# Performance work log

Measured on AMD Instinct MI355X. Metric: run time of the kernel, lower is better.

## Reference

```python
import jax, jax.numpy as jnp
import numpy as np

N = 50000
E = 800000
IN_C = 128
HID = 64
HEADS = 4
EPS = 1e-5
NEG_SLOPE = 0.2


def _glorot(key, shape, fan_in):
    return jax.random.normal(key, shape, dtype=jnp.float32) / np.sqrt(fan_in)


def setup_inputs() -> dict:
    key = jax.random.key(0)
    ks = jax.random.split(key, 32)
    d = {}
    d["x"] = jax.random.normal(ks[0], (N, IN_C), dtype=jnp.float32)
    d["edge_index"] = jax.random.randint(ks[1], (2, E), 0, N, dtype=jnp.int32)
    ph = HID // HEADS  # per-head channels for concat layers (16)
    # Layer 1: in -> [heads, ph], concat
    d["W1"] = _glorot(ks[2], (IN_C, HEADS * ph), IN_C)
    d["a1s"] = _glorot(ks[3], (HEADS, ph), ph)
    d["a1d"] = _glorot(ks[4], (HEADS, ph), ph)
    d["b1"] = jnp.zeros((HID,), jnp.float32)
    # Layer 2: hid -> [heads, ph], concat
    d["W2"] = _glorot(ks[5], (HID, HEADS * ph), HID)
    d["a2s"] = _glorot(ks[6], (HEADS, ph), ph)
    d["a2d"] = _glorot(ks[7], (HEADS, ph), ph)
    d["b2"] = jnp.zeros((HID,), jnp.float32)
    # Layer 3: hid -> [heads, HID], mean over heads (concat=False)
    d["W3"] = _glorot(ks[8], (HID, HEADS * HID), HID)
    d["a3s"] = _glorot(ks[9], (HEADS, HID), HID)
    d["a3d"] = _glorot(ks[10], (HEADS, HID), HID)
    d["b3"] = jnp.zeros((HID,), jnp.float32)
    # BatchNorms (eval mode: running stats)
    for i, k0 in zip((1, 2, 3), (11, 14, 17)):
        d[f"bn{i}_g"] = jnp.ones((HID,), jnp.float32)
        d[f"bn{i}_b"] = jnp.zeros((HID,), jnp.float32)
        d[f"bn{i}_m"] = 0.1 * jax.random.normal(ks[k0], (HID,), dtype=jnp.float32)
        d[f"bn{i}_v"] = jax.random.uniform(ks[k0 + 1], (HID,), minval=0.5, maxval=1.5, dtype=jnp.float32)
    # Classifier MLP: HID -> HID//2 -> 1
    d["cW1"] = _glorot(ks[20], (HID, HID // 2), HID)
    d["cb1"] = jnp.zeros((HID // 2,), jnp.float32)
    d["cW2"] = _glorot(ks[21], (HID // 2, 1), HID // 2)
    d["cb2"] = jnp.zeros((1,), jnp.float32)
    return d


def _gat_layer(x, src, dst, W, a_s, a_d, b, concat):
    n = x.shape[0]
    heads, outc = a_s.shape
    h = (x @ W).reshape(n, heads, outc)           # [N,H,C]
    al_s = jnp.einsum("nhc,hc->nh", h, a_s)       # [N,H]
    al_d = jnp.einsum("nhc,hc->nh", h, a_d)
    e = jax.nn.leaky_relu(al_s[src] + al_d[dst], NEG_SLOPE)  # [E,H]
    m = jax.ops.segment_max(e, dst, num_segments=n)
    ex = jnp.exp(e - m[dst])
    den = jax.ops.segment_sum(ex, dst, num_segments=n)
    alpha = ex / den[dst]                          # segment softmax over dst
    out = jax.ops.segment_sum(h[src] * alpha[..., None], dst, num_segments=n)  # [N,H,C]
    if concat:
        out = out.reshape(n, heads * outc)
    else:
        out = out.mean(axis=1)
    return out + b


def _bn(x, g, b, m, v):
    return g * (x - m) * jax.lax.rsqrt(v + EPS) + b


def reference(x, edge_index, W1, a1s, a1d, b1, W2, a2s, a2d, b2, W3, a3s, a3d, b3,
              bn1_g, bn1_b, bn1_m, bn1_v, bn2_g, bn2_b, bn2_m, bn2_v,
              bn3_g, bn3_b, bn3_m, bn3_v, cW1, cb1, cW2, cb2):
    n = x.shape[0]
    # PyG GATConv adds self-loops by default
    loop = jnp.arange(n, dtype=edge_index.dtype)
    src = jnp.concatenate([edge_index[0], loop])
    dst = jnp.concatenate([edge_index[1], loop])

    h = _gat_layer(x, src, dst, W1, a1s, a1d, b1, concat=True)
    h = jax.nn.elu(_bn(h, bn1_g, bn1_b, bn1_m, bn1_v))
    h = _gat_layer(h, src, dst, W2, a2s, a2d, b2, concat=True)
    h = jax.nn.elu(_bn(h, bn2_g, bn2_b, bn2_m, bn2_v))
    h = _gat_layer(h, src, dst, W3, a3s, a3d, b3, concat=False)
    h = _bn(h, bn3_g, bn3_b, bn3_m, bn3_v)

    h = jax.nn.elu(h @ cW1 + cb1)
    out = (h @ cW2 + cb2).squeeze(-1)  # [N]
    return out
```

## Files before the change

kernel.cpp:

```cpp
#include <hip/hip_runtime.h>

#define HH 4

__device__ __forceinline__ float lrelu(float v){ return v > 0.f ? v : 0.2f*v; }

template<int IC>
__global__ void gemm_gat(const float* __restrict__ X, const float* __restrict__ W,
                         const float* __restrict__ a_s, const float* __restrict__ a_d,
                         float* __restrict__ h, float* __restrict__ als, float* __restrict__ ald,
                         int N) {
    int t = threadIdx.x, lane = t & 63, wid = t >> 6;
    int n = blockIdx.x*4 + wid;
    bool valid = n < N;
    int nc = valid ? n : N-1;
    __shared__ float xs[4][IC];
    #pragma unroll
    for (int k = lane; k < IC; k += 64) xs[wid][k] = X[(size_t)nc*IC + k];
    float acc = 0.f;
    #pragma unroll 8
    for (int k = 0; k < IC; ++k) acc += xs[wid][k] * W[k*64 + lane];
    if (valid) h[(size_t)nc*64 + lane] = acc;
    int hh = lane >> 4, c = lane & 15;
    float ps = acc * a_s[hh*16 + c];
    float pd = acc * a_d[hh*16 + c];
    #pragma unroll
    for (int m = 1; m < 16; m <<= 1){ ps += __shfl_xor(ps, m); pd += __shfl_xor(pd, m); }
    if (valid && c == 0){ als[nc*HH + hh] = ps; ald[nc*HH + hh] = pd; }
}


__global__ void zero_i32(int* __restrict__ p, int n){
    int i = blockIdx.x*256 + threadIdx.x;
    if (i < n) p[i] = 0;
}

__global__ void count_deg(const int* __restrict__ ei, int* __restrict__ deg, int E){
    int e = blockIdx.x*256 + threadIdx.x;
    if (e < E) atomicAdd(&deg[ei[E + e]], 1);
}

__global__ void deg_bsum(const int* __restrict__ deg, int* __restrict__ bsum, int N){
    int t = threadIdx.x;
    int base = blockIdx.x*1024 + t*4;
    int s = 0;
    if (base + 3 < N){
        int4 v = *(const int4*)(deg + base);
        s = v.x + v.y + v.z + v.w;
    } else {
        for (int q = 0; q < 4; ++q) if (base + q < N) s += deg[base + q];
    }
    #pragma unroll
    for (int m = 1; m < 64; m <<= 1) s += __shfl_xor(s, m);
    __shared__ int ws[4];
    if ((t & 63) == 0) ws[t >> 6] = s;
    __syncthreads();
    if (t == 0) bsum[blockIdx.x] = ws[0] + ws[1] + ws[2] + ws[3];
}

__global__ void scan_write(const int* __restrict__ deg, const int* __restrict__ bsum,
                           int* __restrict__ row_off, int* __restrict__ cursor, int N, int E){
    int t = threadIdx.x, bid = blockIdx.x, lane = t & 63, w = t >> 6;
    int base = bid*1024 + t*4;
    int v0 = 0, v1 = 0, v2 = 0, v3 = 0;
    if (base + 3 < N){
        int4 v = *(const int4*)(deg + base);
        v0 = v.x; v1 = v.y; v2 = v.z; v3 = v.w;
    } else {
        if (base     < N) v0 = deg[base];
        if (base + 1 < N) v1 = deg[base + 1];
        if (base + 2 < N) v2 = deg[base + 2];
        if (base + 3 < N) v3 = deg[base + 3];
    }
    int s = v0 + v1 + v2 + v3;
    int x = s;
    #pragma unroll
    for (int d = 1; d < 64; d <<= 1){
        int y = __shfl_up(x, d);
        if (lane >= d) x += y;
    }
    __shared__ int wsum[4];
    __shared__ int boff_s;
    if (lane == 63) wsum[w] = x;
    if (t < 64){
        int o = 0;
        for (int i = t; i < bid; i += 64) o += bsum[i];
        #pragma unroll
        for (int m = 1; m < 64; m <<= 1) o += __shfl_xor(o, m);
        if (t == 0) boff_s = o;
    }
    __syncthreads();
    int woff = 0;
    for (int i = 0; i < w; ++i) woff += wsum[i];
    int o = boff_s + woff + (x - s);
    if (base     < N){ row_off[base]     = o; cursor[base]     = o; o += v0; }
    if (base + 1 < N){ row_off[base + 1] = o; cursor[base + 1] = o; o += v1; }
    if (base + 2 < N){ row_off[base + 2] = o; cursor[base + 2] = o; o += v2; }
    if (base + 3 < N){ row_off[base + 3] = o; cursor[base + 3] = o; o += v3; }
    if (t == 0 && bid == 0) row_off[N] = E;
}

__global__ void fill_csr(const int* __restrict__ ei, int* __restrict__ cursor,
                         int* __restrict__ ssrc, int E){
    int e = blockIdx.x*256 + threadIdx.x;
    if (e < E){
        int d = ei[E + e];
        int p = atomicAdd(&cursor[d], 1);
        ssrc[p] = ei[e];
    }
}

__global__ void prep_l3(const float* __restrict__ W3, const float* __restrict__ a3s,
                        const float* __restrict__ a3d, float* __restrict__ ws3,
                        float* __restrict__ wd3, float* __restrict__ W3p){
    int t = threadIdx.x;
    int hh = t >> 6, k = t & 63;
    float ss = 0.f, sd = 0.f;
    for (int c = 0; c < 64; ++c){
        float w = W3[k*256 + hh*64 + c];
        ss += w * a3s[hh*64 + c];
        sd += w * a3d[hh*64 + c];
        W3p[t*64 + c] = 0.25f * w;
    }
    ws3[t] = ss; wd3[t] = sd;
}

template<bool L3PREP>
__global__ void gat_agg16(const int* __restrict__ row_off, const int* __restrict__ ssrc,
                          const float* __restrict__ als, const float* __restrict__ ald,
                          const float* __restrict__ h, const float* __restrict__ b,
                          const float* __restrict__ g, const float* __restrict__ bb,
                          const float* __restrict__ bm, const float* __restrict__ bv,
                          float* __restrict__ out,
                          const float* __restrict__ ws3, const float* __restrict__ wd3,
                          float* __restrict__ als3, float* __restrict__ ald3, int N){
    int lane = threadIdx.x & 63;
    int n = blockIdx.x*4 + (threadIdx.x >> 6);
    if (n >= N) return;
    int hh = lane >> 4, j = lane & 15, grp = lane & 48;
    float ad = ald[n*HH + hh];
    float vself = __expf(lrelu(als[n*HH + hh] + ad));
    int beg = row_off[n], end = row_off[n+1];
    float denp = 0.f;
    float acc = vself * h[(size_t)n*64 + lane];
    for (int cb = beg; cb < end; cb += 16){
        int e = cb + j;
        int s = n; float ev = 0.f;
        if (e < end){ s = ssrc[e]; ev = __expf(lrelu(als[s*HH + hh] + ad)); }
        denp += ev;
        #pragma unroll
        for (int qb = 0; qb < 16; qb += 8){
            int sq[8]; float hv[8];
            #pragma unroll
            for (int i = 0; i < 8; ++i) sq[i] = __shfl(s, grp | (qb + i));
            #pragma unroll
            for (int i = 0; i < 8; ++i) hv[i] = h[(size_t)sq[i]*64 + lane];
            #pragma unroll
            for (int i = 0; i < 8; ++i) acc += __shfl(ev, grp | (qb + i)) * hv[i];
        }
    }
    #pragma unroll
    for (int m = 1; m < 16; m <<= 1) denp += __shfl_xor(denp, m);
    float den = vself + denp;
    float val = acc/den + b[lane];
    val = g[lane]*(val - bm[lane])*rsqrtf(bv[lane] + 1e-5f) + bb[lane];
    val = val > 0.f ? val : expm1f(val);
    out[(size_t)n*64 + lane] = val;
    if (L3PREP){
        #pragma unroll
        for (int jj = 0; jj < 4; ++jj){
            float ps = val * ws3[jj*64 + lane];
            float pd = val * wd3[jj*64 + lane];
            #pragma unroll
            for (int mm = 1; mm < 64; mm <<= 1){
                ps += __shfl_xor(ps, mm);
                pd += __shfl_xor(pd, mm);
            }
            if (lane == 0){ als3[n*HH + jj] = ps; ald3[n*HH + jj] = pd; }
        }
    }
}

__global__ void gat_agg3_fused(const int* __restrict__ row_off, const int* __restrict__ ssrc,
                               const float* __restrict__ als, const float* __restrict__ ald,
                               const float* __restrict__ hin, const float* __restrict__ W3p,
                               const float* __restrict__ b, const float* __restrict__ g,
                               const float* __restrict__ bb, const float* __restrict__ bm,
                               const float* __restrict__ bv, float* __restrict__ out, int N){
    int t = threadIdx.x, lane = t & 63, wid = t >> 6;
    int n0 = blockIdx.x*4;
    int n = min(n0 + wid, N-1);
    __shared__ __align__(16) float4 wlds[4][64];
    __shared__ int slds[4][64];
    __shared__ __align__(16) float ysh[4*256];
    __shared__ float red[4][4][64];
    float4 adv = *(const float4*)(ald + n*4);
    float4 av  = *(const float4*)(als + n*4);
    float v0 = __expf(lrelu(av.x + adv.x)), v1 = __expf(lrelu(av.y + adv.y));
    float v2 = __expf(lrelu(av.z + adv.z)), v3 = __expf(lrelu(av.w + adv.w));
    int beg = row_off[n], end = row_off[n+1];
    float hv0 = hin[(size_t)n*64 + lane];
    float acc0 = v0*hv0, acc1 = v1*hv0, acc2 = v2*hv0, acc3 = v3*hv0;
    float dp0 = 0.f, dp1 = 0.f, dp2 = 0.f, dp3 = 0.f;
    for (int cb = beg; cb < end; cb += 64){
        int e = cb + lane;
        int s = n; float e0 = 0.f, e1 = 0.f, e2 = 0.f, e3 = 0.f;
        if (e < end){
            s = ssrc[e];
            float4 a = *(const float4*)(als + s*4);
            e0 = __expf(lrelu(a.x + adv.x));
            e1 = __expf(lrelu(a.y + adv.y));
            e2 = __expf(lrelu(a.z + adv.z));
            e3 = __expf(lrelu(a.w + adv.w));
        }
        dp0 += e0; dp1 += e1; dp2 += e2; dp3 += e3;
        wlds[wid][lane] = make_float4(e0, e1, e2, e3);
        slds[wid][lane] = s;
        int cn = min(64, end - cb);
        for (int qb = 0; qb < cn; qb += 8){
            int sq[8]; float hv[8]; float4 wv[8];
            #pragma unroll
            for (int i = 0; i < 8; ++i) sq[i] = slds[wid][qb + i];
            #pragma unroll
            for (int i = 0; i < 8; ++i) hv[i] = hin[(size_t)sq[i]*64 + lane];
            #pragma unroll
            for (int i = 0; i < 8; ++i) wv[i] = wlds[wid][qb + i];
            #pragma unroll
            for (int i = 0; i < 8; ++i){
                acc0 += wv[i].x*hv[i];
                acc1 += wv[i].y*hv[i];
                acc2 += wv[i].z*hv[i];
                acc3 += wv[i].w*hv[i];
            }
        }
    }
    #pragma unroll
    for (int m = 1; m < 64; m <<= 1){
        dp0 += __shfl_xor(dp0, m); dp1 += __shfl_xor(dp1, m);
        dp2 += __shfl_xor(dp2, m); dp3 += __shfl_xor(dp3, m);
    }
    ysh[wid*256 +   0 + lane] = acc0/(v0 + dp0);
    ysh[wid*256 +  64 + lane] = acc1/(v1 + dp1);
    ysh[wid*256 + 128 + lane] = acc2/(v2 + dp2);
    ysh[wid*256 + 192 + lane] = acc3/(v3 + dp3);
    __syncthreads();
    float a0 = 0.f, a1 = 0.f, a2 = 0.f, a3 = 0.f;
    int jbase = wid*64;
    #pragma unroll 4
    for (int jj = 0; jj < 64; jj += 4){
        int jb = jbase + jj;
        float4 y0 = *(const float4*)&ysh[0*256 + jb];
        float4 y1 = *(const float4*)&ysh[1*256 + jb];
        float4 y2 = *(const float4*)&ysh[2*256 + jb];
        float4 y3 = *(const float4*)&ysh[3*256 + jb];
        float w0 = W3p[(jb    )*64 + lane];
        float w1 = W3p[(jb + 1)*64 + lane];
        float w2 = W3p[(jb + 2)*64 + lane];
        float w3 = W3p[(jb + 3)*64 + lane];
        a0 += y0.x*w0 + y0.y*w1 + y0.z*w2 + y0.w*w3;
        a1 += y1.x*w0 + y1.y*w1 + y1.z*w2 + y1.w*w3;
        a2 += y2.x*w0 + y2.y*w1 + y2.z*w2 + y2.w*w3;
        a3 += y3.x*w0 + y3.y*w1 + y3.z*w2 + y3.w*w3;
    }
    red[wid][0][lane] = a0;
    red[wid][1][lane] = a1;
    red[wid][2][lane] = a2;
    red[wid][3][lane] = a3;
    __syncthreads();
    int nw = n0 + wid;
    if (nw < N){
        float val = red[0][wid][lane] + red[1][wid][lane] +
                    red[2][wid][lane] + red[3][wid][lane] + b[lane];
        out[(size_t)nw*64 + lane] = g[lane]*(val - bm[lane])*rsqrtf(bv[lane] + 1e-5f) + bb[lane];
    }
}

__global__ void classifier(const float* __restrict__ hin, const float* __restrict__ cW1,
                           const float* __restrict__ cb1, const float* __restrict__ cW2,
                           const float* __restrict__ cb2, float* __restrict__ out, int N){
    __shared__ float w1[64*32];
    __shared__ float b1s[32], w2[32];
    int t = threadIdx.x;
    for (int k = t; k < 64*32; k += 256) w1[k] = cW1[k];
    if (t < 32) { b1s[t] = cb1[t]; w2[t] = cW2[t]; }
    __syncthreads();
    int n = blockIdx.x*256 + t;
    if (n >= N) return;
    float hrow[64];
    #pragma unroll
    for (int k = 0; k < 64; ++k) hrow[k] = hin[(size_t)n*64 + k];
    float acc2 = cb2[0];
    #pragma unroll 4
    for (int j = 0; j < 32; ++j) {
        float a = b1s[j];
        #pragma unroll
        for (int k = 0; k < 64; ++k) a += hrow[k]*w1[k*32 + j];
        float e = a > 0.f ? a : expm1f(a);
        acc2 += e * w2[j];
    }
    out[n] = acc2;
}

extern "C" void kernel_launch(void* const* d_in, const int* in_sizes, int n_in,
                              void* d_out, int out_size, void* d_ws, size_t ws_size,
                              hipStream_t stream) {
    const float* x    = (const float*)d_in[0];
    const int*   ei   = (const int*)  d_in[1];
    const float* W1   = (const float*)d_in[2];
    const float* a1s  = (const float*)d_in[3];
    const float* a1d  = (const float*)d_in[4];
    const float* b1   = (const float*)d_in[5];
    const float* W2   = (const float*)d_in[6];
    const float* a2s  = (const float*)d_in[7];
    const float* a2d  = (const float*)d_in[8];
    const float* b2   = (const float*)d_in[9];
    const float* W3   = (const float*)d_in[10];
    const float* a3s  = (const float*)d_in[11];
    const float* a3d  = (const float*)d_in[12];
    const float* b3   = (const float*)d_in[13];
    const float* bn1g = (const float*)d_in[14];
    const float* bn1b = (const float*)d_in[15];
    const float* bn1m = (const float*)d_in[16];
    const float* bn1v = (const float*)d_in[17];
    const float* bn2g = (const float*)d_in[18];
    const float* bn2b = (const float*)d_in[19];
    const float* bn2m = (const float*)d_in[20];
    const float* bn2v = (const float*)d_in[21];
    const float* bn3g = (const float*)d_in[22];
    const float* bn3b = (const float*)d_in[23];
    const float* bn3m = (const float*)d_in[24];
    const float* bn3v = (const float*)d_in[25];
    const float* cW1  = (const float*)d_in[26];
    const float* cb1  = (const float*)d_in[27];
    const float* cW2  = (const float*)d_in[28];
    const float* cb2  = (const float*)d_in[29];

    const int N = in_sizes[0] / 128;
    const int E = in_sizes[1] / 2;

    float* h    = (float*)d_ws;
    float* hin  = h    + (size_t)N*64;
    float* als  = hin  + (size_t)N*64;
    float* ald  = als  + (size_t)N*4;
    float* als3 = ald  + (size_t)N*4;
    float* ald3 = als3 + (size_t)N*4;
    float* ws3  = ald3 + (size_t)N*4;
    float* wd3  = ws3  + 256;
    float* W3p  = wd3  + 256;
    int* deg     = (int*)(W3p + 16384);
    int* row_off = deg + N;
    int* cursor  = row_off + (N + 1);
    int* ssrc    = cursor + N;
    int* bsum    = ssrc + E;

    const int B = 256;
    int gN  = (N + B-1)/B;
    int gE  = (E + B-1)/B;
    int NB  = (N + 1023)/1024;
    int gN4 = (N + 3)/4;

    zero_i32<<<gN, B, 0, stream>>>(deg, N);
    count_deg<<<gE, B, 0, stream>>>(ei, deg, E);
    deg_bsum<<<NB, B, 0, stream>>>(deg, bsum, N);
    scan_write<<<NB, B, 0, stream>>>(deg, bsum, row_off, cursor, N, E);
    fill_csr<<<gE, B, 0, stream>>>(ei, cursor, ssrc, E);
    prep_l3<<<1, 256, 0, stream>>>(W3, a3s, a3d, ws3, wd3, W3p);

    gemm_gat<128><<<gN4, B, 0, stream>>>(x, W1, a1s, a1d, h, als, ald, N);
    gat_agg16<false><<<gN4, B, 0, stream>>>(row_off, ssrc, als, ald, h, b1,
                                            bn1g, bn1b, bn1m, bn1v, hin,
                                            nullptr, nullptr, nullptr, nullptr, N);

    gemm_gat<64><<<gN4, B, 0, stream>>>(hin, W2, a2s, a2d, h, als, ald, N);
    gat_agg16<true><<<gN4, B, 0, stream>>>(row_off, ssrc, als, ald, h, b2,
                                           bn2g, bn2b, bn2m, bn2v, hin,
                                           ws3, wd3, als3, ald3, N);

    gat_agg3_fused<<<gN4, B, 0, stream>>>(row_off, ssrc, als3, ald3, hin, W3p,
                                          b3, bn3g, bn3b, bn3m, bn3v, h, N);

    classifier<<<gN, B, 0, stream>>>(h, cW1, cb1, cW2, cb2, (float*)d_out, N);
}
```

Before: 401.6 us.

## Gather neighbor features as float4 with four edges per wavefront in parallel

The aggregation kernels for layers 1/2 and layer 3 now split each wavefront into four 16-lane groups. Each group loads a different neighbor's 64-float row as float4 vectors, so four edges are processed at once instead of one edge per 64-lane row load. Partial accumulators are combined afterwards with cross-group shuffles. The aim is fewer, wider gather instructions and more memory-level parallelism, at the cost of extra shuffle reductions and LDS staging of edge weights.

```diff
diff --git a/kernel.cpp b/kernel.cpp
--- a/kernel.cpp
+++ b/kernel.cpp
@@ -133,50 +133,74 @@
                           float* __restrict__ out,
                           const float* __restrict__ ws3, const float* __restrict__ wd3,
                           float* __restrict__ als3, float* __restrict__ ald3, int N){
-    int lane = threadIdx.x & 63;
-    int n = blockIdx.x*4 + (threadIdx.x >> 6);
+    int t = threadIdx.x, lane = t & 63, wid = t >> 6;
+    int n = blockIdx.x*4 + wid;
     if (n >= N) return;
-    int hh = lane >> 4, j = lane & 15, grp = lane & 48;
-    float ad = ald[n*HH + hh];
-    float vself = __expf(lrelu(als[n*HH + hh] + ad));
+    __shared__ float wl[4][16][4];
+    __shared__ int   sl[4][16];
+    int j  = lane & 15;
+    int hh = lane >> 4;
+    int cb = lane & 15;
+    int gq = lane >> 4;
+    int hd = cb >> 2;
+    float ad_w = ald[n*HH + hh];
+    float v_hd = __expf(lrelu(als[n*HH + hd] + ald[n*HH + hd]));
     int beg = row_off[n], end = row_off[n+1];
+    float4 acc = make_float4(0.f, 0.f, 0.f, 0.f);
+    if (lane < 16){
+        float4 hs = *(const float4*)(h + (size_t)n*64 + cb*4);
+        acc.x = v_hd*hs.x; acc.y = v_hd*hs.y; acc.z = v_hd*hs.z; acc.w = v_hd*hs.w;
+    }
     float denp = 0.f;
-    float acc = vself * h[(size_t)n*64 + lane];
-    for (int cb = beg; cb < end; cb += 16){
-        int e = cb + j;
+    for (int c16 = beg; c16 < end; c16 += 16){
+        int e = c16 + j;
         int s = n; float ev = 0.f;
-        if (e < end){ s = ssrc[e]; ev = __expf(lrelu(als[s*HH + hh] + ad)); }
+        if (e < end){ s = ssrc[e]; ev = __expf(lrelu(als[s*HH + hh] + ad_w)); }
         denp += ev;
+        wl[wid][j][hh] = ev;
+        if (hh == 0) sl[wid][j] = s;
+        int cnt = min(16, end - c16);
+        for (int qb = 0; qb < cnt; qb += 8){
+            int eA = qb + gq, eB = qb + 4 + gq;
+            int   sA = sl[wid][eA],     sB = sl[wid][eB];
+            float wA = wl[wid][eA][hd], wB = wl[wid][eB][hd];
+            float4 hA = *(const float4*)(h + (size_t)sA*64 + cb*4);
+            float4 hB = *(const float4*)(h + (size_t)sB*64 + cb*4);
+            acc.x += wA*hA.x; acc.y += wA*hA.y; acc.z += wA*hA.z; acc.w += wA*hA.w;
+            acc.x += wB*hB.x; acc.y += wB*hB.y; acc.z += wB*hB.z; acc.w += wB*hB.w;
+        }
+    }
+    #pragma unroll
+    for (int m = 1; m < 16; m <<= 1) denp += __shfl_xor(denp, m);
+    float den = __shfl(denp, hd << 4) + v_hd;
+    #pragma unroll
+    for (int m = 16; m < 64; m <<= 1){
+        acc.x += __shfl_xor(acc.x, m); acc.y += __shfl_xor(acc.y, m);
+        acc.z += __shfl_xor(acc.z, m); acc.w += __shfl_xor(acc.w, m);
+    }
+    float4 bb4 = *(const float4*)(b  + cb*4);
+    float4 gg4 = *(const float4*)(g  + cb*4);
+    float4 be4 = *(const float4*)(bb + cb*4);
+    float4 bm4 = *(const float4*)(bm + cb*4);
+    float4 bv4 = *(const float4*)(bv + cb*4);
+    float4 val;
+    val.x = gg4.x*(acc.x/den + bb4.x - bm4.x)*rsqrtf(bv4.x + 1e-5f) + be4.x;
+    val.y = gg4.y*(acc.y/den + bb4.y - bm4.y)*rsqrtf(bv4.y + 1e-5f) + be4.y;
+    val.z = gg4.z*(acc.z/den + bb4.z - bm4.z)*rsqrtf(bv4.z + 1e-5f) + be4.z;
+    val.w = gg4.w*(acc.w/den + bb4.w - bm4.w)*rsqrtf(bv4.w + 1e-5f) + be4.w;
+    val.x = val.x > 0.f ? val.x : expm1f(val.x);
+    val.y = val.y > 0.f ? val.y : expm1f(val.y);
+    val.z = val.z > 0.f ? val.z : expm1f(val.z);
+    val.w = val.w > 0.f ? val.w : expm1f(val.w);
+    if (lane < 16) *(float4*)(out + (size_t)n*64 + cb*4) = val;
+    if (L3PREP){
+        float4 w_s = *(const float4*)(ws3 + gq*64 + cb*4);
+        float4 w_d = *(const float4*)(wd3 + gq*64 + cb*4);
+        float ps = val.x*w_s.x + val.y*w_s.y + val.z*w_s.z + val.w*w_s.w;
+        float pd = val.x*w_d.x + val.y*w_d.y + val.z*w_d.z + val.w*w_d.w;
         #pragma unroll
-        for (int qb = 0; qb < 16; qb += 8){
-            int sq[8]; float hv[8];
-            #pragma unroll
-            for (int i = 0; i < 8; ++i) sq[i] = __shfl(s, grp | (qb + i));
-            #pragma unroll
-            for (int i = 0; i < 8; ++i) hv[i] = h[(size_t)sq[i]*64 + lane];
-            #pragma unroll
-            for (int i = 0; i < 8; ++i) acc += __shfl(ev, grp | (qb + i)) * hv[i];
-        }
-    }
-    #pragma unroll
-    for (int m = 1; m < 16; m <<= 1) denp += __shfl_xor(denp, m);
-    float den = vself + denp;
-    float val = acc/den + b[lane];
-    val = g[lane]*(val - bm[lane])*rsqrtf(bv[lane] + 1e-5f) + bb[lane];
-    val = val > 0.f ? val : expm1f(val);
-    out[(size_t)n*64 + lane] = val;
-    if (L3PREP){
-        #pragma unroll
-        for (int jj = 0; jj < 4; ++jj){
-            float ps = val * ws3[jj*64 + lane];
-            float pd = val * wd3[jj*64 + lane];
-            #pragma unroll
-            for (int mm = 1; mm < 64; mm <<= 1){
-                ps += __shfl_xor(ps, mm);
-                pd += __shfl_xor(pd, mm);
-            }
-            if (lane == 0){ als3[n*HH + jj] = ps; ald3[n*HH + jj] = pd; }
-        }
+        for (int m = 1; m < 16; m <<= 1){ ps += __shfl_xor(ps, m); pd += __shfl_xor(pd, m); }
+        if (cb == 0){ als3[n*HH + gq] = ps; ald3[n*HH + gq] = pd; }
     }
 }
 
@@ -193,16 +217,23 @@
     __shared__ int slds[4][64];
     __shared__ __align__(16) float ysh[4*256];
     __shared__ float red[4][4][64];
+    int cb = lane & 15, gq = lane >> 4;
     float4 adv = *(const float4*)(ald + n*4);
     float4 av  = *(const float4*)(als + n*4);
     float v0 = __expf(lrelu(av.x + adv.x)), v1 = __expf(lrelu(av.y + adv.y));
     float v2 = __expf(lrelu(av.z + adv.z)), v3 = __expf(lrelu(av.w + adv.w));
     int beg = row_off[n], end = row_off[n+1];
-    float hv0 = hin[(size_t)n*64 + lane];
-    float acc0 = v0*hv0, acc1 = v1*hv0, acc2 = v2*hv0, acc3 = v3*hv0;
+    float4 acc0 = make_float4(0,0,0,0), acc1 = acc0, acc2 = acc0, acc3 = acc0;
+    if (lane < 16){
+        float4 hs = *(const float4*)(hin + (size_t)n*64 + cb*4);
+        acc0.x = v0*hs.x; acc0.y = v0*hs.y; acc0.z = v0*hs.z; acc0.w = v0*hs.w;
+        acc1.x = v1*hs.x; acc1.y = v1*hs.y; acc1.z = v1*hs.z; acc1.w = v1*hs.w;
+        acc2.x = v2*hs.x; acc2.y = v2*hs.y; acc2.z = v2*hs.z; acc2.w = v2*hs.w;
+        acc3.x = v3*hs.x; acc3.y = v3*hs.y; acc3.z = v3*hs.z; acc3.w = v3*hs.w;
+    }
     float dp0 = 0.f, dp1 = 0.f, dp2 = 0.f, dp3 = 0.f;
-    for (int cb = beg; cb < end; cb += 64){
-        int e = cb + lane;
+    for (int c64 = beg; c64 < end; c64 += 64){
+        int e = c64 + lane;
         int s = n; float e0 = 0.f, e1 = 0.f, e2 = 0.f, e3 = 0.f;
         if (e < end){
             s = ssrc[e];
@@ -215,22 +246,21 @@
         dp0 += e0; dp1 += e1; dp2 += e2; dp3 += e3;
         wlds[wid][lane] = make_float4(e0, e1, e2, e3);
         slds[wid][lane] = s;
-        int cn = min(64, end - cb);
+        int cn = min(64, end - c64);
         for (int qb = 0; qb < cn; qb += 8){
-            int sq[8]; float hv[8]; float4 wv[8];
-            #pragma unroll
-            for (int i = 0; i < 8; ++i) sq[i] = slds[wid][qb + i];
-            #pragma unroll
-            for (int i = 0; i < 8; ++i) hv[i] = hin[(size_t)sq[i]*64 + lane];
-            #pragma unroll
-            for (int i = 0; i < 8; ++i) wv[i] = wlds[wid][qb + i];
-            #pragma unroll
-            for (int i = 0; i < 8; ++i){
-                acc0 += wv[i].x*hv[i];
-                acc1 += wv[i].y*hv[i];
-                acc2 += wv[i].z*hv[i];
-                acc3 += wv[i].w*hv[i];
-            }
+            int eA = qb + gq, eB = qb + 4 + gq;
+            int sA = slds[wid][eA], sB = slds[wid][eB];
+            float4 wA = wlds[wid][eA], wB = wlds[wid][eB];
+            float4 hA = *(const float4*)(hin + (size_t)sA*64 + cb*4);
+            float4 hB = *(const float4*)(hin + (size_t)sB*64 + cb*4);
+            acc0.x += wA.x*hA.x; acc0.y += wA.x*hA.y; acc0.z += wA.x*hA.z; acc0.w += wA.x*hA.w;
+            acc1.x += wA.y*hA.x; acc1.y += wA.y*hA.y; acc1.z += wA.y*hA.z; acc1.w += wA.y*hA.w;
+            acc2.x += wA.z*hA.x; acc2.y += wA.z*hA.y; acc2.z += wA.z*hA.z; acc2.w += wA.z*hA.w;
+            acc3.x += wA.w*hA.x; acc3.y += wA.w*hA.y; acc3.z += wA.w*hA.z; acc3.w += wA.w*hA.w;
+            acc0.x += wB.x*hB.x; acc0.y += wB.x*hB.y; acc0.z += wB.x*hB.z; acc0.w += wB.x*hB.w;
+            acc1.x += wB.y*hB.x; acc1.y += wB.y*hB.y; acc1.z += wB.y*hB.z; acc1.w += wB.y*hB.w;
+            acc2.x += wB.z*hB.x; acc2.y += wB.z*hB.y; acc2.z += wB.z*hB.z; acc2.w += wB.z*hB.w;
+            acc3.x += wB.w*hB.x; acc3.y += wB.w*hB.y; acc3.z += wB.w*hB.z; acc3.w += wB.w*hB.w;
         }
     }
     #pragma unroll
@@ -238,10 +268,29 @@
         dp0 += __shfl_xor(dp0, m); dp1 += __shfl_xor(dp1, m);
         dp2 += __shfl_xor(dp2, m); dp3 += __shfl_xor(dp3, m);
     }
-    ysh[wid*256 +   0 + lane] = acc0/(v0 + dp0);
-    ysh[wid*256 +  64 + lane] = acc1/(v1 + dp1);
-    ysh[wid*256 + 128 + lane] = acc2/(v2 + dp2);
-    ysh[wid*256 + 192 + lane] = acc3/(v3 + dp3);
+    #pragma unroll
+    for (int m = 16; m < 64; m <<= 1){
+        acc0.x += __shfl_xor(acc0.x, m); acc0.y += __shfl_xor(acc0.y, m);
+        acc0.z += __shfl_xor(acc0.z, m); acc0.w += __shfl_xor(acc0.w, m);
+        acc1.x += __shfl_xor(acc1.x, m); acc1.y += __shfl_xor(acc1.y, m);
+        acc1.z += __shfl_xor(acc1.z, m); acc1.w += __shfl_xor(acc1.w, m);
+        acc2.x += __shfl_xor(acc2.x, m); acc2.y += __shfl_xor(acc2.y, m);
+        acc2.z += __shfl_xor(acc2.z, m); acc2.w += __shfl_xor(acc2.w, m);
+        acc3.x += __shfl_xor(acc3.x, m); acc3.y += __shfl_xor(acc3.y, m);
+        acc3.z += __shfl_xor(acc3.z, m); acc3.w += __shfl_xor(acc3.w, m);
+    }
+    if (lane < 16){
+        float r0 = 1.f/(v0 + dp0), r1 = 1.f/(v1 + dp1);
+        float r2 = 1.f/(v2 + dp2), r3 = 1.f/(v3 + dp3);
+        float4 y0 = make_float4(acc0.x*r0, acc0.y*r0, acc0.z*r0, acc0.w*r0);
+        float4 y1 = make_float4(acc1.x*r1, acc1.y*r1, acc1.z*r1, acc1.w*r1);
+        float4 y2 = make_float4(acc2.x*r2, acc2.y*r2, acc2.z*r2, acc2.w*r2);
+        float4 y3 = make_float4(acc3.x*r3, acc3.y*r3, acc3.z*r3, acc3.w*r3);
+        *(float4*)&ysh[wid*256 +   0 + cb*4] = y0;
+        *(float4*)&ysh[wid*256 +  64 + cb*4] = y1;
+        *(float4*)&ysh[wid*256 + 128 + cb*4] = y2;
+        *(float4*)&ysh[wid*256 + 192 + cb*4] = y3;
+    }
     __syncthreads();
     float a0 = 0.f, a1 = 0.f, a2 = 0.f, a3 = 0.f;
     int jbase = wid*64;
```

Result: faster. 386.5 us (-3.8%).
